# Optimization experiments

Hardware: AMD Instinct MI355X
Metric: run time of the kernel (lower is better)

## Reference

```python
import jax, jax.numpy as jnp
import numpy as np


def _gru(x, Wih, Whh, bih, bhh):
    """Single-layer torch-style GRU, batch_first. x:[B,T,E], Wih:[3H,E], Whh:[3H,H]."""
    gi = jnp.einsum('bte,ge->btg', x, Wih) + bih  # precompute input gates [B,T,3H]
    H = Whh.shape[1]
    h0 = jnp.zeros((x.shape[0], H), x.dtype)

    def step(h, gi_t):
        gh = h @ Whh.T + bhh
        i_r, i_z, i_n = jnp.split(gi_t, 3, axis=-1)
        h_r, h_z, h_n = jnp.split(gh, 3, axis=-1)
        r = jax.nn.sigmoid(i_r + h_r)
        z = jax.nn.sigmoid(i_z + h_z)
        n = jnp.tanh(i_n + r * h_n)
        h_new = (1.0 - z) * n + z * h
        return h_new, h_new

    _, hs = jax.lax.scan(step, h0, jnp.swapaxes(gi, 0, 1))
    return jnp.swapaxes(hs, 0, 1)  # [B,T,H]


def setup_inputs() -> dict:
    V, E, H, B, S, Tc, Ts = 100000, 256, 256, 256, 10, 20, 50
    Bc = B * S
    k = jax.random.split(jax.random.key(0), 16)
    w = lambda kk, shp, s=0.05: (jax.random.normal(kk, shp) * s).astype(jnp.float32)
    return {
        'input_cate_batch': jax.random.randint(k[0], (Bc, Tc), 0, V),
        'mask_cate_batch': jnp.ones((Bc, Tc), jnp.float32),
        'mask_cate_seq_batch': jnp.ones((B, S), jnp.float32),
        'max_actionNum_cate_batch': Tc,
        'max_subseqNum_cate_batch': S,
        'subseqLen_cate_batch': jax.random.randint(k[1], (Bc,), 0, Tc),
        'seqLen_cate_batch': jax.random.randint(k[2], (B,), 0, S),
        'input_batch': jax.random.randint(k[3], (B, Ts), 0, V),
        'mask_batch': jnp.ones((B, Ts), jnp.float32),
        'seqLen_batch': jax.random.randint(k[4], (B,), 0, Ts),
        'target_y_batch': jax.random.randint(k[5], (B,), 0, V),
        'train_test_flag': 0,
        'emb': w(k[6], (V, E), 0.02),
        'Wih_c': w(k[7], (3 * H, E)), 'Whh_c': w(k[8], (3 * H, H)),
        'bih_c': jnp.zeros((3 * H,), jnp.float32), 'bhh_c': jnp.zeros((3 * H,), jnp.float32),
        'Wih_s': w(k[9], (3 * H, E)), 'Whh_s': w(k[10], (3 * H, H)),
        'bih_s': jnp.zeros((3 * H,), jnp.float32), 'bhh_s': jnp.zeros((3 * H,), jnp.float32),
        'fc_W': w(k[11], (H, 2 * H)), 'fc_b': jnp.zeros((H,), jnp.float32),
    }


def reference(input_cate_batch, mask_cate_batch, mask_cate_seq_batch,
              max_actionNum_cate_batch, max_subseqNum_cate_batch,
              subseqLen_cate_batch, seqLen_cate_batch, input_batch, mask_batch,
              seqLen_batch, target_y_batch, train_test_flag,
              emb, Wih_c, Whh_c, bih_c, bhh_c, Wih_s, Whh_s, bih_s, bhh_s,
              fc_W, fc_b):
    Bc = input_cate_batch.shape[0]
    B = input_batch.shape[0]
    S = max_subseqNum_cate_batch
    # --- category GRU over subsequences ---
    x_c = emb[input_cate_batch]                                  # [Bc,Tc,E]
    out_c = _gru(x_c, Wih_c, Whh_c, bih_c, bhh_c) * mask_cate_batch[:, :, None]
    gathered = out_c[jnp.arange(Bc), subseqLen_cate_batch]       # [Bc,H] per-row length gather
    seq_cate = gathered.reshape(B, S, -1)                        # [B,S,H]
    # --- short GRU over the recent session ---
    x_s = emb[input_batch]                                       # [B,Ts,E]
    out_s = _gru(x_s, Wih_s, Whh_s, bih_s, bhh_s) * mask_batch[:, :, None]
    out_short = out_s[jnp.arange(B), seqLen_batch]               # [B,H]
    # --- masked softmax attention of short state over subseq states ---
    att = jnp.einsum('bsh,bh->bs', seq_cate, out_short)          # [B,S]
    w = jax.nn.softmax(att, axis=1) * mask_cate_seq_batch
    w = w / jnp.sum(w, axis=1, keepdims=True)
    sum_cate = jnp.einsum('bs,bsh->bh', w, seq_cate)             # [B,H]
    mix = jnp.concatenate([sum_cate, out_short], axis=1)         # [B,2H]
    fc_out = mix @ fc_W.T + fc_b                                 # [B,H]
    logits = fc_out @ emb.T                                      # [B,V] shared-embedding output layer
    return logits, target_y_batch
```

## Files before the change

kernel.cpp:

```cpp
#include <hip/hip_runtime.h>
#include <cmath>

#define EMB_V 100000
#define BATCH 256
#define SUBS  10
#define BC    2560
#define TC    20
#define TS    50

using bf16x8 = __attribute__((ext_vector_type(8))) short;
using f32x4  = __attribute__((ext_vector_type(4))) float;

__device__ __forceinline__ unsigned short f2bf(float f) {
    unsigned int u = __float_as_uint(f);
    u += 0x7fff + ((u >> 16) & 1);
    return (unsigned short)(u >> 16);
}
__device__ __forceinline__ float bf2f(unsigned short u) {
    return __uint_as_float(((unsigned int)u) << 16);
}
__device__ __forceinline__ float sigmoid_fast(float x) {
    return __builtin_amdgcn_rcpf(1.f + __expf(-x));
}
__device__ __forceinline__ float tanh_fast(float x) {
    float e = __expf(2.f * x);
    return 1.f - 2.f * __builtin_amdgcn_rcpf(e + 1.f);
}

__global__ void transpose_rm(const float* __restrict__ in, float* __restrict__ out,
                             int rows, int cols) {
    int o = blockIdx.x * 256 + threadIdx.x;
    if (o >= rows * cols) return;
    int c = o / rows;
    int r = o - c * rows;
    out[o] = in[r * cols + c];
}

__global__ void f32_to_bf16(const float* __restrict__ in, unsigned short* __restrict__ out,
                            int n4) {
    for (int i = blockIdx.x * 256 + threadIdx.x; i < n4; i += gridDim.x * 256) {
        float4 v = ((const float4*)in)[i];
        ((ushort4*)out)[i] = make_ushort4(f2bf(v.x), f2bf(v.y), f2bf(v.z), f2bf(v.w));
    }
}

__global__ void pack_whh(const float* __restrict__ W, unsigned short* __restrict__ P) {
    int t = blockIdx.x * 256 + threadIdx.x;
    if (t >= 48 * 8 * 64) return;
    int l = t & 63, kc = (t >> 6) & 7, nt = t >> 9;
    int g = nt % 3, cg = nt / 3;
    int n = g * 256 + cg * 16 + (l & 15);
    int k = kc * 32 + (l >> 4) * 8;
    const float* src = W + n * 256 + k;
    unsigned short* dst = P + (size_t)t * 8;
#pragma unroll
    for (int j = 0; j < 8; ++j) dst[j] = f2bf(src[j]);
}

template <bool GATHER, bool OBF16, bool NGUARD>
__global__ __launch_bounds__(256, 2) void gemm_abt(
    const unsigned short* __restrict__ A, const int* __restrict__ tok,
    const unsigned short* __restrict__ B, void* __restrict__ Cout,
    int N, int ldc)
{
    __shared__ unsigned short Asub[128][72];
    __shared__ unsigned short Bsub[128][72];
    const int tid = threadIdx.x;
    const int l = tid & 63, wave = tid >> 6;
    const int lm = l & 15, quad = l >> 4;
    const int wm = wave >> 1, wn = wave & 1;
    const int n0 = blockIdx.x * 128, m0 = blockIdx.y * 128;

    f32x4 acc[4][4];
#pragma unroll
    for (int mi = 0; mi < 4; ++mi)
#pragma unroll
        for (int ni = 0; ni < 4; ++ni) acc[mi][ni] = (f32x4){0.f, 0.f, 0.f, 0.f};

    for (int kk = 0; kk < 4; ++kk) {
        const int k0 = kk * 64;
#pragma unroll
        for (int i = 0; i < 4; ++i) {
            int slot = tid + i * 256;
            int row = slot >> 3, g8 = (slot & 7) * 8;
            const unsigned short* src = GATHER
                ? A + (size_t)tok[m0 + row] * 256 + k0 + g8
                : A + (size_t)(m0 + row) * 256 + k0 + g8;
            *(bf16x8*)&Asub[row][g8] = *(const bf16x8*)src;
        }
#pragma unroll
        for (int i = 0; i < 4; ++i) {
            int slot = tid + i * 256;
            int row = slot >> 3, g8 = (slot & 7) * 8;
            int n = n0 + row;
            bf16x8 v = {0, 0, 0, 0, 0, 0, 0, 0};
            if (!NGUARD || n < N) v = *(const bf16x8*)(B + (size_t)n * 256 + k0 + g8);
            *(bf16x8*)&Bsub[row][g8] = v;
        }
        __syncthreads();
#pragma unroll
        for (int kc = 0; kc < 2; ++kc) {
            bf16x8 af[4], bfv[4];
#pragma unroll
            for (int mi = 0; mi < 4; ++mi)
                af[mi] = *(const bf16x8*)&Asub[wm * 64 + mi * 16 + lm][kc * 32 + quad * 8];
#pragma unroll
            for (int ni = 0; ni < 4; ++ni)
                bfv[ni] = *(const bf16x8*)&Bsub[wn * 64 + ni * 16 + lm][kc * 32 + quad * 8];
#pragma unroll
            for (int mi = 0; mi < 4; ++mi)
#pragma unroll
                for (int ni = 0; ni < 4; ++ni)
                    acc[mi][ni] = __builtin_amdgcn_mfma_f32_16x16x32_bf16(
                        af[mi], bfv[ni], acc[mi][ni], 0, 0, 0);
        }
        __syncthreads();
    }
#pragma unroll
    for (int mi = 0; mi < 4; ++mi)
#pragma unroll
        for (int ni = 0; ni < 4; ++ni) {
            int col = n0 + wn * 64 + ni * 16 + lm;
            if (NGUARD && col >= N) continue;
#pragma unroll
            for (int i = 0; i < 4; ++i) {
                int row = m0 + wm * 64 + mi * 16 + quad * 4 + i;
                if (OBF16)
                    ((unsigned short*)Cout)[(size_t)row * ldc + col] = f2bf(acc[mi][ni][i]);
                else
                    ((float*)Cout)[(size_t)row * ldc + col] = acc[mi][ni][i];
            }
        }
}

__global__ __launch_bounds__(512, 2) void gru_scan_fused(
    const unsigned short* __restrict__ gi_c, const unsigned short* __restrict__ pW_c,
    const float* __restrict__ bih_c, const float* __restrict__ bhh_c,
    const int* __restrict__ len_c, const float* __restrict__ mask_c,
    float* __restrict__ out_c,
    const unsigned short* __restrict__ gi_s, const unsigned short* __restrict__ pW_s,
    const float* __restrict__ bih_s, const float* __restrict__ bhh_s,
    const int* __restrict__ len_s, const float* __restrict__ mask_s,
    float* __restrict__ out_s)
{
    __shared__ unsigned short h_lds[2][16][264];
    __shared__ unsigned short b_lds[8 * 17 * 512];

    const bool is_cat = blockIdx.x < (BC / 16);
    const int  T      = is_cat ? TC : TS;
    const int  row0   = (is_cat ? blockIdx.x : blockIdx.x - BC / 16) * 16;
    const unsigned short* gi   = is_cat ? gi_c  : gi_s;
    const unsigned short* pW   = is_cat ? pW_c  : pW_s;
    const float*          bih  = is_cat ? bih_c : bih_s;
    const float*          bhh  = is_cat ? bhh_c : bhh_s;
    const int*            lenp = is_cat ? len_c : len_s;
    const float*          mask = is_cat ? mask_c : mask_s;
    float*                outp = is_cat ? out_c : out_s;

    const int tid  = threadIdx.x;
    const int l    = tid & 63, w = tid >> 6;
    const int lm   = l & 15,   quad = l >> 4;

    for (int i = tid; i < 2 * 16 * 264; i += 512) ((unsigned short*)h_lds)[i] = 0;

    bf16x8 breg[31];
#pragma unroll
    for (int ti = 0; ti < 6; ++ti)
#pragma unroll
        for (int kc = 0; kc < 8; ++kc) {
            bf16x8 v = *((const bf16x8*)pW + (size_t)((6 * w + ti) * 8 + kc) * 64 + l);
            if ((ti == 0) ? (kc < 6) : (kc < 5)) {
                breg[(ti == 0) ? kc : 6 + (ti - 1) * 5 + kc] = v;
            } else {
                int slot = (ti == 0) ? (kc - 6) : 2 + (ti - 1) * 3 + (kc - 5);
                *(bf16x8*)&b_lds[((w * 17 + slot) * 64 + l) * 8] = v;
            }
        }

    const int c0 = 32 * w + lm, c1 = c0 + 16;
    const float cR0 = bih[c0] + bhh[c0],             cR1 = bih[c1] + bhh[c1];
    const float cZ0 = bih[256 + c0] + bhh[256 + c0], cZ1 = bih[256 + c1] + bhh[256 + c1];
    const float cNi0 = bih[512 + c0], cNi1 = bih[512 + c1];
    const float cNh0 = bhh[512 + c0], cNh1 = bhh[512 + c1];

    int len[4];
    const unsigned short* gpa[4];
#pragma unroll
    for (int i = 0; i < 4; ++i) {
        const int r = quad * 4 + i;
        len[i] = lenp[row0 + r];
        gpa[i] = gi + (size_t)(row0 + r) * T * 768 + c0;
    }

    float hold0[4] = {0.f, 0.f, 0.f, 0.f};
    float hold1[4] = {0.f, 0.f, 0.f, 0.f};

    __syncthreads();

    for (int t = 0; t < T; ++t) {
        unsigned short g00[4], g01[4], g02[4], g10[4], g11[4], g12[4];
#pragma unroll
        for (int i = 0; i < 4; ++i) {
            const unsigned short* p = gpa[i];
            g00[i] = p[0];  g01[i] = p[256]; g02[i] = p[512];
            g10[i] = p[16]; g11[i] = p[272]; g12[i] = p[528];
            gpa[i] = p + 768;
        }

        const unsigned short (*hb)[264] = h_lds[t & 1];
        bf16x8 a[8];
#pragma unroll
        for (int kc = 0; kc < 8; ++kc)
            a[kc] = *(const bf16x8*)&hb[lm][kc * 32 + quad * 8];

        f32x4 acc[6];
#pragma unroll
        for (int ti = 0; ti < 6; ++ti) acc[ti] = (f32x4){0.f, 0.f, 0.f, 0.f};
#pragma unroll
        for (int ti = 0; ti < 6; ++ti)
#pragma unroll
            for (int kc = 0; kc < 8; ++kc) {
                bf16x8 b;
                if ((ti == 0) ? (kc < 6) : (kc < 5)) {
                    b = breg[(ti == 0) ? kc : 6 + (ti - 1) * 5 + kc];
                } else {
                    int slot = (ti == 0) ? (kc - 6) : 2 + (ti - 1) * 3 + (kc - 5);
                    b = *(const bf16x8*)&b_lds[((w * 17 + slot) * 64 + l) * 8];
                }
                acc[ti] = __builtin_amdgcn_mfma_f32_16x16x32_bf16(a[kc], b, acc[ti], 0, 0, 0);
            }

        unsigned short (*hw)[264] = h_lds[(t + 1) & 1];
#pragma unroll
        for (int i = 0; i < 4; ++i) {
            const int r = quad * 4 + i;
            {
                float rg = sigmoid_fast(bf2f(g00[i]) + acc[0][i] + cR0);
                float zg = sigmoid_fast(bf2f(g01[i]) + acc[1][i] + cZ0);
                float ng = tanh_fast(bf2f(g02[i]) + cNi0 + rg * (acc[2][i] + cNh0));
                float hn = zg * (hold0[i] - ng) + ng;
                hold0[i] = hn;
                hw[r][c0] = f2bf(hn);
                if (t == len[i])
                    outp[(size_t)(row0 + r) * 256 + c0] = hn * mask[(row0 + r) * T + t];
            }
            {
                float rg = sigmoid_fast(bf2f(g10[i]) + acc[3][i] + cR1);
                float zg = sigmoid_fast(bf2f(g11[i]) + acc[4][i] + cZ1);
                float ng = tanh_fast(bf2f(g12[i]) + cNi1 + rg * (acc[5][i] + cNh1));
                float hn = zg * (hold1[i] - ng) + ng;
                hold1[i] = hn;
                hw[r][c1] = f2bf(hn);
                if (t == len[i])
                    outp[(size_t)(row0 + r) * 256 + c1] = hn * mask[(row0 + r) * T + t];
            }
        }

        asm volatile("s_waitcnt lgkmcnt(0)" ::: "memory");
        __builtin_amdgcn_sched_barrier(0);
        __builtin_amdgcn_s_barrier();
        __builtin_amdgcn_sched_barrier(0);
    }
}

__global__ __launch_bounds__(256) void attn_fc(
    const float* __restrict__ seq_cate, const float* __restrict__ out_short,
    const float* __restrict__ mask_seq, const float* __restrict__ fcWT,
    const float* __restrict__ fc_b, const int* __restrict__ target,
    unsigned short* __restrict__ fc_out, float* __restrict__ d_out)
{
    __shared__ float sc[SUBS][256];
    __shared__ float os[256];
    __shared__ float part[SUBS][256];
    __shared__ float mix[512];
    const int b = blockIdx.x, tid = threadIdx.x;

    os[tid] = out_short[b * 256 + tid];
    for (int s = 0; s < SUBS; ++s) sc[s][tid] = seq_cate[(size_t)(b * SUBS + s) * 256 + tid];
    __syncthreads();

    for (int s = 0; s < SUBS; ++s) part[s][tid] = sc[s][tid] * os[tid];
    __syncthreads();
    for (int off = 128; off >= 1; off >>= 1) {
        if (tid < off)
            for (int s = 0; s < SUBS; ++s) part[s][tid] += part[s][tid + off];
        __syncthreads();
    }

    float w[SUBS];
    float m = -1e30f;
    for (int s = 0; s < SUBS; ++s) m = fmaxf(m, part[s][0]);
    float sum = 0.f;
    for (int s = 0; s < SUBS; ++s) { w[s] = __expf(part[s][0] - m); sum += w[s]; }
    float tot = 0.f;
    for (int s = 0; s < SUBS; ++s) { w[s] = (w[s] / sum) * mask_seq[b * SUBS + s]; tot += w[s]; }
    float inv = 1.f / tot;

    float sumc = 0.f;
    for (int s = 0; s < SUBS; ++s) sumc += w[s] * inv * sc[s][tid];
    mix[tid] = sumc;
    mix[256 + tid] = os[tid];
    __syncthreads();

    float acc = fc_b[tid];
    for (int jj = 0; jj < 512; ++jj) acc = fmaf(mix[jj], fcWT[jj * 256 + tid], acc);
    fc_out[b * 256 + tid] = f2bf(acc);

    if (tid == 0) d_out[(size_t)BATCH * EMB_V + b] = (float)target[b];
}

extern "C" void kernel_launch(void* const* d_in, const int* in_sizes, int n_in,
                              void* d_out, int out_size, void* d_ws, size_t ws_size,
                              hipStream_t stream) {
    const int*   input_cate   = (const int*)d_in[0];
    const float* mask_cate    = (const float*)d_in[1];
    const float* mask_seq     = (const float*)d_in[2];
    const int*   subseqLen    = (const int*)d_in[5];
    const int*   input_batch  = (const int*)d_in[7];
    const float* mask_batch   = (const float*)d_in[8];
    const int*   seqLen_batch = (const int*)d_in[9];
    const int*   target       = (const int*)d_in[10];
    const float* emb          = (const float*)d_in[12];
    const float* Wih_c        = (const float*)d_in[13];
    const float* Whh_c        = (const float*)d_in[14];
    const float* bih_c        = (const float*)d_in[15];
    const float* bhh_c        = (const float*)d_in[16];
    const float* Wih_s        = (const float*)d_in[17];
    const float* Whh_s        = (const float*)d_in[18];
    const float* bih_s        = (const float*)d_in[19];
    const float* bhh_s        = (const float*)d_in[20];
    const float* fc_W         = (const float*)d_in[21];
    const float* fc_b         = (const float*)d_in[22];
    float* out = (float*)d_out;

    float* ws = (float*)d_ws;
    float*          fcWT      = ws;
    float*          out_short = ws + 131072;
    unsigned short* fc_outb   = (unsigned short*)(ws + 196608);
    float*          seq_cate  = ws + 229376;
    unsigned short* packW_c   = (unsigned short*)(ws + 884736);
    unsigned short* packW_s   = (unsigned short*)(ws + 983040);
    unsigned short* wihb_c    = (unsigned short*)(ws + 1081344);
    unsigned short* wihb_s    = (unsigned short*)(ws + 1179648);
    unsigned short* embb      = (unsigned short*)(ws + 1277952);
    unsigned short* gi_c      = (unsigned short*)(ws + 14077952);
    unsigned short* gi_s      = (unsigned short*)(ws + 33738752);

    transpose_rm<<<512, 256, 0, stream>>>(fc_W, fcWT, 256, 512);
    pack_whh<<<96, 256, 0, stream>>>(Whh_c, packW_c);
    pack_whh<<<96, 256, 0, stream>>>(Whh_s, packW_s);

    f32_to_bf16<<<2048, 256, 0, stream>>>(emb, embb, EMB_V * 256 / 4);
    f32_to_bf16<<<192, 256, 0, stream>>>(Wih_c, wihb_c, 768 * 256 / 4);
    f32_to_bf16<<<192, 256, 0, stream>>>(Wih_s, wihb_s, 768 * 256 / 4);

    gemm_abt<true, true, false><<<dim3(6, 400), 256, 0, stream>>>(
        embb, input_cate, wihb_c, gi_c, 768, 768);
    gemm_abt<true, true, false><<<dim3(6, 100), 256, 0, stream>>>(
        embb, input_batch, wihb_s, gi_s, 768, 768);

    gru_scan_fused<<<BC / 16 + BATCH / 16, 512, 0, stream>>>(
        gi_c, packW_c, bih_c, bhh_c, subseqLen, mask_cate, seq_cate,
        gi_s, packW_s, bih_s, bhh_s, seqLen_batch, mask_batch, out_short);

    attn_fc<<<BATCH, 256, 0, stream>>>(
        seq_cate, out_short, mask_seq, fcWT, fc_b, target, fc_outb, out);

    gemm_abt<false, false, true><<<dim3(782, 2), 256, 0, stream>>>(
        fc_outb, nullptr, embb, out, EMB_V, EMB_V);
}
```

Measured before the change: 459.7 us.

## Use direct global-to-LDS loads in GEMM and GRU, merge prep kernels

The GEMM now stages A and B tiles with global_load_lds 16-byte direct copies into unpadded LDS, precomputes gather offsets, and raises launch bounds to three blocks per CU. The GRU scan now double-buffers each timestep's input-gate rows into LDS with async direct loads, instead of scalar per-lane global reads on the critical path. It also keeps more recurrent weights in registers and reorders the MFMA loop by k-chunk. Several small weight-prep kernels are merged into one launch. The risks are LDS bank conflicts from dropping the padding, higher LDS use in the scan lowering occupancy, and the output GEMM losing its N bound guard on B loads, so edge tiles read past the embedding table into adjacent workspace.

```diff
diff --git a/kernel.cpp b/kernel.cpp
--- a/kernel.cpp
+++ b/kernel.cpp
@@ -26,26 +26,13 @@
     float e = __expf(2.f * x);
     return 1.f - 2.f * __builtin_amdgcn_rcpf(e + 1.f);
 }
-
-__global__ void transpose_rm(const float* __restrict__ in, float* __restrict__ out,
-                             int rows, int cols) {
-    int o = blockIdx.x * 256 + threadIdx.x;
-    if (o >= rows * cols) return;
-    int c = o / rows;
-    int r = o - c * rows;
-    out[o] = in[r * cols + c];
-}
-
-__global__ void f32_to_bf16(const float* __restrict__ in, unsigned short* __restrict__ out,
-                            int n4) {
-    for (int i = blockIdx.x * 256 + threadIdx.x; i < n4; i += gridDim.x * 256) {
-        float4 v = ((const float4*)in)[i];
-        ((ushort4*)out)[i] = make_ushort4(f2bf(v.x), f2bf(v.y), f2bf(v.z), f2bf(v.w));
-    }
-}
-
-__global__ void pack_whh(const float* __restrict__ W, unsigned short* __restrict__ P) {
-    int t = blockIdx.x * 256 + threadIdx.x;
+__device__ __forceinline__ void dma16(const void* g, void* l) {
+    __builtin_amdgcn_global_load_lds((const __attribute__((address_space(1))) void*)g,
+                                     (__attribute__((address_space(3))) void*)l, 16, 0, 0);
+}
+
+__device__ __forceinline__ void pack_whh_dev(const float* __restrict__ W,
+                                             unsigned short* __restrict__ P, int t) {
     if (t >= 48 * 8 * 64) return;
     int l = t & 63, kc = (t >> 6) & 7, nt = t >> 9;
     int g = nt % 3, cg = nt / 3;
@@ -56,21 +43,64 @@
 #pragma unroll
     for (int j = 0; j < 8; ++j) dst[j] = f2bf(src[j]);
 }
+__global__ __launch_bounds__(256) void prep_misc(
+    const float* __restrict__ fc_W, float* __restrict__ fcWT,
+    const float* __restrict__ Whh_c, unsigned short* __restrict__ packW_c,
+    const float* __restrict__ Whh_s, unsigned short* __restrict__ packW_s,
+    const float* __restrict__ Wih_c, unsigned short* __restrict__ wihb_c,
+    const float* __restrict__ Wih_s, unsigned short* __restrict__ wihb_s)
+{
+    const int b = blockIdx.x, tid = threadIdx.x;
+    if (b < 512) {
+        int o = b * 256 + tid;
+        int c = o >> 8, r = o & 255;
+        fcWT[o] = fc_W[r * 512 + c];
+    } else if (b < 608) {
+        pack_whh_dev(Whh_c, packW_c, (b - 512) * 256 + tid);
+    } else if (b < 704) {
+        pack_whh_dev(Whh_s, packW_s, (b - 608) * 256 + tid);
+    } else if (b < 896) {
+        int i = (b - 704) * 256 + tid;
+        float4 v = ((const float4*)Wih_c)[i];
+        ((ushort4*)wihb_c)[i] = make_ushort4(f2bf(v.x), f2bf(v.y), f2bf(v.z), f2bf(v.w));
+    } else {
+        int i = (b - 896) * 256 + tid;
+        float4 v = ((const float4*)Wih_s)[i];
+        ((ushort4*)wihb_s)[i] = make_ushort4(f2bf(v.x), f2bf(v.y), f2bf(v.z), f2bf(v.w));
+    }
+}
+
+__global__ void f32_to_bf16(const float* __restrict__ in, unsigned short* __restrict__ out,
+                            int n4) {
+    for (int i = blockIdx.x * 256 + threadIdx.x; i < n4; i += gridDim.x * 256) {
+        float4 v = ((const float4*)in)[i];
+        ((ushort4*)out)[i] = make_ushort4(f2bf(v.x), f2bf(v.y), f2bf(v.z), f2bf(v.w));
+    }
+}
 
 template <bool GATHER, bool OBF16, bool NGUARD>
-__global__ __launch_bounds__(256, 2) void gemm_abt(
+__global__ __launch_bounds__(256, 3) void gemm_abt(
     const unsigned short* __restrict__ A, const int* __restrict__ tok,
     const unsigned short* __restrict__ B, void* __restrict__ Cout,
     int N, int ldc)
 {
-    __shared__ unsigned short Asub[128][72];
-    __shared__ unsigned short Bsub[128][72];
+    __shared__ unsigned short Asub[128 * 64];
+    __shared__ unsigned short Bsub[128 * 64];
     const int tid = threadIdx.x;
     const int l = tid & 63, wave = tid >> 6;
     const int lm = l & 15, quad = l >> 4;
     const int wm = wave >> 1, wn = wave & 1;
     const int n0 = blockIdx.x * 128, m0 = blockIdx.y * 128;
 
+    unsigned aofs[4], bofs[4];
+#pragma unroll
+    for (int i = 0; i < 4; ++i) {
+        int c = tid + i * 256, row = c >> 3, cc = c & 7;
+        aofs[i] = (GATHER ? (unsigned)tok[m0 + row] : (unsigned)(m0 + row)) * 256u + cc * 8u;
+        bofs[i] = (unsigned)(n0 + row) * 256u + cc * 8u;
+    }
+    const int dstu = (tid & 192) * 8;
+
     f32x4 acc[4][4];
 #pragma unroll
     for (int mi = 0; mi < 4; ++mi)
@@ -80,33 +110,21 @@
     for (int kk = 0; kk < 4; ++kk) {
         const int k0 = kk * 64;
 #pragma unroll
-        for (int i = 0; i < 4; ++i) {
-            int slot = tid + i * 256;
-            int row = slot >> 3, g8 = (slot & 7) * 8;
-            const unsigned short* src = GATHER
-                ? A + (size_t)tok[m0 + row] * 256 + k0 + g8
-                : A + (size_t)(m0 + row) * 256 + k0 + g8;
-            *(bf16x8*)&Asub[row][g8] = *(const bf16x8*)src;
-        }
-#pragma unroll
-        for (int i = 0; i < 4; ++i) {
-            int slot = tid + i * 256;
-            int row = slot >> 3, g8 = (slot & 7) * 8;
-            int n = n0 + row;
-            bf16x8 v = {0, 0, 0, 0, 0, 0, 0, 0};
-            if (!NGUARD || n < N) v = *(const bf16x8*)(B + (size_t)n * 256 + k0 + g8);
-            *(bf16x8*)&Bsub[row][g8] = v;
-        }
+        for (int i = 0; i < 4; ++i)
+            dma16(A + aofs[i] + k0, &Asub[dstu + i * 2048]);
+#pragma unroll
+        for (int i = 0; i < 4; ++i)
+            dma16(B + bofs[i] + k0, &Bsub[dstu + i * 2048]);
         __syncthreads();
 #pragma unroll
         for (int kc = 0; kc < 2; ++kc) {
             bf16x8 af[4], bfv[4];
 #pragma unroll
             for (int mi = 0; mi < 4; ++mi)
-                af[mi] = *(const bf16x8*)&Asub[wm * 64 + mi * 16 + lm][kc * 32 + quad * 8];
+                af[mi] = *(const bf16x8*)&Asub[(wm * 64 + mi * 16 + lm) * 64 + kc * 32 + quad * 8];
 #pragma unroll
             for (int ni = 0; ni < 4; ++ni)
-                bfv[ni] = *(const bf16x8*)&Bsub[wn * 64 + ni * 16 + lm][kc * 32 + quad * 8];
+                bfv[ni] = *(const bf16x8*)&Bsub[(wn * 64 + ni * 16 + lm) * 64 + kc * 32 + quad * 8];
 #pragma unroll
             for (int mi = 0; mi < 4; ++mi)
 #pragma unroll
@@ -144,7 +162,8 @@
     float* __restrict__ out_s)
 {
     __shared__ unsigned short h_lds[2][16][264];
-    __shared__ unsigned short b_lds[8 * 17 * 512];
+    __shared__ unsigned short b_lds[8 * 4 * 512];
+    __shared__ unsigned short gi_lds[2][16 * 768];
 
     const bool is_cat = blockIdx.x < (BC / 16);
     const int  T      = is_cat ? TC : TS;
@@ -163,18 +182,15 @@
 
     for (int i = tid; i < 2 * 16 * 264; i += 512) ((unsigned short*)h_lds)[i] = 0;
 
-    bf16x8 breg[31];
+    bf16x8 breg[44];
 #pragma unroll
     for (int ti = 0; ti < 6; ++ti)
 #pragma unroll
         for (int kc = 0; kc < 8; ++kc) {
             bf16x8 v = *((const bf16x8*)pW + (size_t)((6 * w + ti) * 8 + kc) * 64 + l);
-            if ((ti == 0) ? (kc < 6) : (kc < 5)) {
-                breg[(ti == 0) ? kc : 6 + (ti - 1) * 5 + kc] = v;
-            } else {
-                int slot = (ti == 0) ? (kc - 6) : 2 + (ti - 1) * 3 + (kc - 5);
-                *(bf16x8*)&b_lds[((w * 17 + slot) * 64 + l) * 8] = v;
-            }
+            if (ti < 5)           breg[ti * 8 + kc] = v;
+            else if (kc < 4)      breg[40 + kc] = v;
+            else *(bf16x8*)&b_lds[((w * 4 + (kc - 4)) * 64 + l) * 8] = v;
         }
 
     const int c0 = 32 * w + lm, c1 = c0 + 16;
@@ -184,12 +200,21 @@
     const float cNh0 = bhh[512 + c0], cNh1 = bhh[512 + c1];
 
     int len[4];
-    const unsigned short* gpa[4];
-#pragma unroll
-    for (int i = 0; i < 4; ++i) {
-        const int r = quad * 4 + i;
-        len[i] = lenp[row0 + r];
-        gpa[i] = gi + (size_t)(row0 + r) * T * 768 + c0;
+#pragma unroll
+    for (int i = 0; i < 4; ++i) len[i] = lenp[row0 + quad * 4 + i];
+
+    const unsigned short* gq[3];
+    const int dstu = (tid & 448) * 8;
+#pragma unroll
+    for (int i = 0; i < 3; ++i) {
+        int c = tid + i * 512;
+        int row = c / 96, cc = c - row * 96;
+        gq[i] = gi + ((size_t)(row0 + row) * T) * 768 + cc * 8;
+    }
+#pragma unroll
+    for (int i = 0; i < 3; ++i) {
+        dma16(gq[i], &gi_lds[0][dstu + i * 8192]);
+        gq[i] += 768;
     }
 
     float hold0[4] = {0.f, 0.f, 0.f, 0.f};
@@ -198,46 +223,41 @@
     __syncthreads();
 
     for (int t = 0; t < T; ++t) {
-        unsigned short g00[4], g01[4], g02[4], g10[4], g11[4], g12[4];
-#pragma unroll
-        for (int i = 0; i < 4; ++i) {
-            const unsigned short* p = gpa[i];
-            g00[i] = p[0];  g01[i] = p[256]; g02[i] = p[512];
-            g10[i] = p[16]; g11[i] = p[272]; g12[i] = p[528];
-            gpa[i] = p + 768;
+        if (t + 1 < T) {
+#pragma unroll
+            for (int i = 0; i < 3; ++i) {
+                dma16(gq[i], &gi_lds[(t + 1) & 1][dstu + i * 8192]);
+                gq[i] += 768;
+            }
         }
 
         const unsigned short (*hb)[264] = h_lds[t & 1];
-        bf16x8 a[8];
-#pragma unroll
-        for (int kc = 0; kc < 8; ++kc)
-            a[kc] = *(const bf16x8*)&hb[lm][kc * 32 + quad * 8];
-
         f32x4 acc[6];
 #pragma unroll
         for (int ti = 0; ti < 6; ++ti) acc[ti] = (f32x4){0.f, 0.f, 0.f, 0.f};
 #pragma unroll
-        for (int ti = 0; ti < 6; ++ti)
-#pragma unroll
-            for (int kc = 0; kc < 8; ++kc) {
+        for (int kc = 0; kc < 8; ++kc) {
+            bf16x8 a = *(const bf16x8*)&hb[lm][kc * 32 + quad * 8];
+#pragma unroll
+            for (int ti = 0; ti < 6; ++ti) {
                 bf16x8 b;
-                if ((ti == 0) ? (kc < 6) : (kc < 5)) {
-                    b = breg[(ti == 0) ? kc : 6 + (ti - 1) * 5 + kc];
-                } else {
-                    int slot = (ti == 0) ? (kc - 6) : 2 + (ti - 1) * 3 + (kc - 5);
-                    b = *(const bf16x8*)&b_lds[((w * 17 + slot) * 64 + l) * 8];
-                }
-                acc[ti] = __builtin_amdgcn_mfma_f32_16x16x32_bf16(a[kc], b, acc[ti], 0, 0, 0);
-            }
-
+                if (ti < 5)           b = breg[ti * 8 + kc];
+                else if (kc < 4)      b = breg[40 + kc];
+                else b = *(const bf16x8*)&b_lds[((w * 4 + (kc - 4)) * 64 + l) * 8];
+                acc[ti] = __builtin_amdgcn_mfma_f32_16x16x32_bf16(a, b, acc[ti], 0, 0, 0);
+            }
+        }
+
+        const unsigned short* gb = gi_lds[t & 1];
         unsigned short (*hw)[264] = h_lds[(t + 1) & 1];
 #pragma unroll
         for (int i = 0; i < 4; ++i) {
             const int r = quad * 4 + i;
+            const unsigned short* gr = gb + r * 768;
             {
-                float rg = sigmoid_fast(bf2f(g00[i]) + acc[0][i] + cR0);
-                float zg = sigmoid_fast(bf2f(g01[i]) + acc[1][i] + cZ0);
-                float ng = tanh_fast(bf2f(g02[i]) + cNi0 + rg * (acc[2][i] + cNh0));
+                float rg = sigmoid_fast(bf2f(gr[c0]) + acc[0][i] + cR0);
+                float zg = sigmoid_fast(bf2f(gr[256 + c0]) + acc[1][i] + cZ0);
+                float ng = tanh_fast(bf2f(gr[512 + c0]) + cNi0 + rg * (acc[2][i] + cNh0));
                 float hn = zg * (hold0[i] - ng) + ng;
                 hold0[i] = hn;
                 hw[r][c0] = f2bf(hn);
@@ -245,9 +265,9 @@
                     outp[(size_t)(row0 + r) * 256 + c0] = hn * mask[(row0 + r) * T + t];
             }
             {
-                float rg = sigmoid_fast(bf2f(g10[i]) + acc[3][i] + cR1);
-                float zg = sigmoid_fast(bf2f(g11[i]) + acc[4][i] + cZ1);
-                float ng = tanh_fast(bf2f(g12[i]) + cNi1 + rg * (acc[5][i] + cNh1));
+                float rg = sigmoid_fast(bf2f(gr[c1]) + acc[3][i] + cR1);
+                float zg = sigmoid_fast(bf2f(gr[256 + c1]) + acc[4][i] + cZ1);
+                float ng = tanh_fast(bf2f(gr[512 + c1]) + cNi1 + rg * (acc[5][i] + cNh1));
                 float hn = zg * (hold1[i] - ng) + ng;
                 hold1[i] = hn;
                 hw[r][c1] = f2bf(hn);
@@ -256,7 +276,7 @@
             }
         }
 
-        asm volatile("s_waitcnt lgkmcnt(0)" ::: "memory");
+        asm volatile("s_waitcnt vmcnt(0) lgkmcnt(0)" ::: "memory");
         __builtin_amdgcn_sched_barrier(0);
         __builtin_amdgcn_s_barrier();
         __builtin_amdgcn_sched_barrier(0);
@@ -346,13 +366,9 @@
     unsigned short* gi_c      = (unsigned short*)(ws + 14077952);
     unsigned short* gi_s      = (unsigned short*)(ws + 33738752);
 
-    transpose_rm<<<512, 256, 0, stream>>>(fc_W, fcWT, 256, 512);
-    pack_whh<<<96, 256, 0, stream>>>(Whh_c, packW_c);
-    pack_whh<<<96, 256, 0, stream>>>(Whh_s, packW_s);
-
+    prep_misc<<<1088, 256, 0, stream>>>(fc_W, fcWT, Whh_c, packW_c, Whh_s, packW_s,
+                                        Wih_c, wihb_c, Wih_s, wihb_s);
     f32_to_bf16<<<2048, 256, 0, stream>>>(emb, embb, EMB_V * 256 / 4);
-    f32_to_bf16<<<192, 256, 0, stream>>>(Wih_c, wihb_c, 768 * 256 / 4);
-    f32_to_bf16<<<192, 256, 0, stream>>>(Wih_s, wihb_s, 768 * 256 / 4);
 
     gemm_abt<true, true, false><<<dim3(6, 400), 256, 0, stream>>>(
         embb, input_cate, wihb_c, gi_c, 768, 768);
```

New measurement: 450.1 us. -2.1%, faster.
